# Optimization experiments

Hardware: AMD Instinct MI355X
Metric: run time of the kernel (lower is better)

## Reference

```python
import jax, jax.numpy as jnp
import numpy as np

B, L, H, NH, NB = 16, 200, 128, 2, 2
ITEMS, SPAN = 50000, 256
NEG = -2.0**32 + 1.0  # mask value used by the torch module


def _ln(x, g, b, eps=1e-8):
    m = jnp.mean(x, axis=-1, keepdims=True)
    v = jnp.mean((x - m) ** 2, axis=-1, keepdims=True)
    return (x - m) / jnp.sqrt(v + eps) * g + b


def setup_inputs() -> dict:
    key = jax.random.key(0)
    ks = jax.random.split(key, 20)
    p = lambda k, s: (jax.random.normal(k, s, jnp.float32) * 0.02)
    item_emb = p(ks[0], (ITEMS + 1, H)).at[0].set(0.0)  # padding_idx=0
    return {
        "user_ids": jax.random.randint(ks[1], (B,), 0, 10000),
        "log_seqs": jax.random.randint(ks[2], (B, L), 0, ITEMS),
        "time_matrices": jax.random.randint(ks[3], (B, L, L), 0, SPAN),
        "pos_seqs": jax.random.randint(ks[4], (B, L), 0, ITEMS),
        "neg_seqs": jax.random.randint(ks[5], (B, L), 0, ITEMS),
        "item_emb": item_emb,
        "pos_K_emb": p(ks[6], (L, H)),
        "pos_V_emb": p(ks[7], (L, H)),
        "time_K_emb": p(ks[8], (SPAN + 1, H)),
        "time_V_emb": p(ks[9], (SPAN + 1, H)),
        "Wq": p(ks[10], (NB, H, H)), "bq": jnp.zeros((NB, H)),
        "Wk": p(ks[11], (NB, H, H)), "bk": jnp.zeros((NB, H)),
        "Wv": p(ks[12], (NB, H, H)), "bv": jnp.zeros((NB, H)),
        "ln1_g": jnp.ones((NB, H)), "ln1_b": jnp.zeros((NB, H)),
        "W1": p(ks[13], (NB, H, H)), "b1": jnp.zeros((NB, H)),
        "W2": p(ks[14], (NB, H, H)), "b2": jnp.zeros((NB, H)),
        "ln2_g": jnp.ones((NB, H)), "ln2_b": jnp.zeros((NB, H)),
        "lnf_g": jnp.ones((H,)), "lnf_b": jnp.zeros((H,)),
    }


def reference(user_ids, log_seqs, time_matrices, pos_seqs, neg_seqs,
              item_emb, pos_K_emb, pos_V_emb, time_K_emb, time_V_emb,
              Wq, bq, Wk, bk, Wv, bv, ln1_g, ln1_b,
              W1, b1, W2, b2, ln2_g, ln2_b, lnf_g, lnf_b):
    d = H // NH
    pad = (log_seqs == 0)                    # (B,L) timeline mask
    keep = (~pad)[..., None].astype(jnp.float32)

    seqs = item_emb[log_seqs] * jnp.sqrt(jnp.float32(H))
    seqs = seqs * keep
    posK = pos_K_emb.reshape(L, NH, d)       # same for every batch element
    posV = pos_V_emb.reshape(L, NH, d)
    tmK = time_K_emb[time_matrices].reshape(B, L, L, NH, d)  # (B,L,L,h,d)
    tmV = time_V_emb[time_matrices].reshape(B, L, L, NH, d)
    causal = ~jnp.tril(jnp.ones((L, L), dtype=bool))          # True = masked
    mask = pad[:, None, :, None] | causal[None, None, :, :]   # (B,1,L,L) row-mask | causal

    for i in range(NB):
        Q = (seqs @ Wq[i].T + bq[i]).reshape(B, L, NH, d)
        K = (seqs @ Wk[i].T + bk[i]).reshape(B, L, NH, d)
        V = (seqs @ Wv[i].T + bv[i]).reshape(B, L, NH, d)
        aw = jnp.einsum('bqhd,bkhd->bhqk', Q, K)
        aw = aw + jnp.einsum('bqhd,khd->bhqk', Q, posK)
        aw = aw + jnp.einsum('bqkhd,bqhd->bhqk', tmK, Q)
        aw = aw / jnp.sqrt(jnp.float32(d))
        aw = jnp.where(mask, NEG, aw)
        A = jax.nn.softmax(aw, axis=-1)                        # (B,h,L,L)
        out = jnp.einsum('bhqk,bkhd->bqhd', A, V)
        out = out + jnp.einsum('bhqk,khd->bqhd', A, posV)
        out = out + jnp.einsum('bhqk,bqkhd->bqhd', A, tmV)
        out = out.reshape(B, L, H)
        seqs = _ln(seqs + out, ln1_g[i], ln1_b[i])
        ffn = jax.nn.relu(seqs @ W1[i].T + b1[i]) @ W2[i].T + b2[i]
        seqs = _ln(seqs + ffn, ln2_g[i], ln2_b[i])
        seqs = seqs * keep

    log_feats = _ln(seqs, lnf_g, lnf_b)
    pos_logits = jnp.sum(log_feats * item_emb[pos_seqs], axis=-1)  # (B,L)
    neg_logits = jnp.sum(log_feats * item_emb[neg_seqs], axis=-1)
    return jnp.stack([pos_logits, neg_logits])  # (2,B,L)
```

## Files before the change

kernel.cpp:

```cpp
#include <hip/hip_runtime.h>
#include <hip/hip_bf16.h>
#include <math.h>

#define BB 16
#define LL 200
#define HH 128
#define DD 64
#define NQT 25
#define NEGF -4294967295.0f
#define SQRTH 11.313708498984761f

__global__ __launch_bounds__(512) void k_qkv(float* __restrict__ seqs,
    const int* __restrict__ log_seqs, const float* __restrict__ item_emb, int do_embed,
    const float* __restrict__ Wq, const float* __restrict__ bq,
    const float* __restrict__ Wk, const float* __restrict__ bk,
    const float* __restrict__ Wv, const float* __restrict__ bv,
    const float* __restrict__ posK, const float* __restrict__ posV,
    float* __restrict__ Q, float* __restrict__ Kp, float* __restrict__ Vp) {
    __shared__ float s_lds[16][HH];
    int r0g = blockIdx.x * 16;
    int t = threadIdx.x;
    if (do_embed) {
        int r = t >> 5, d4 = t & 31;
        int id = log_seqs[r0g + r];
        float4 v = make_float4(0.f, 0.f, 0.f, 0.f);
        if (id != 0) {
            v = ((const float4*)(item_emb + id * HH))[d4];
            v.x *= SQRTH; v.y *= SQRTH; v.z *= SQRTH; v.w *= SQRTH;
        }
        *(float4*)&s_lds[r][d4 * 4] = v;
        ((float4*)(seqs + r0g * HH))[t] = v;
    } else {
        ((float4*)s_lds)[t] = ((const float4*)(seqs + r0g * HH))[t];
    }
    __syncthreads();
    int c = t & 127, rg = t >> 7;
    float aq[4] = {0.f, 0.f, 0.f, 0.f};
    float ak[4] = {0.f, 0.f, 0.f, 0.f};
    float av[4] = {0.f, 0.f, 0.f, 0.f};
    const float4* wq4 = (const float4*)(Wq + c * HH);
    const float4* wk4 = (const float4*)(Wk + c * HH);
    const float4* wv4 = (const float4*)(Wv + c * HH);
#pragma unroll 4
    for (int k4 = 0; k4 < HH / 4; ++k4) {
        float4 wq = wq4[k4], wk = wk4[k4], wv = wv4[k4];
#pragma unroll
        for (int r = 0; r < 4; ++r) {
            float4 s = *(const float4*)&s_lds[rg * 4 + r][k4 * 4];
            aq[r] += s.x * wq.x + s.y * wq.y + s.z * wq.z + s.w * wq.w;
            ak[r] += s.x * wk.x + s.y * wk.y + s.z * wk.z + s.w * wk.w;
            av[r] += s.x * wv.x + s.y * wv.y + s.z * wv.z + s.w * wv.w;
        }
    }
#pragma unroll
    for (int r = 0; r < 4; ++r) {
        int row = r0g + rg * 4 + r;
        int l = row % LL;
        Q[row * HH + c]  = aq[r] + bq[c];
        Kp[row * HH + c] = ak[r] + bk[c] + posK[l * HH + c];
        Vp[row * HH + c] = av[r] + bv[c] + posV[l * HH + c];
    }
}

__global__ __launch_bounds__(256) void k_proj(const float* __restrict__ Q,
    const float* __restrict__ timeK, float* __restrict__ projK) {
    int bh = blockIdx.x / 25, qt = blockIdx.x % 25;
    int b = bh >> 1, h = bh & 1;
    int qlo = qt * 8;
    __shared__ float Qs[8][68];
    __shared__ float TK[2][32][68];
    int t = threadIdx.x;
    if (t < 128) {
        int r = t >> 4, d4 = t & 15;
        *(float4*)&Qs[r][d4 * 4] =
            ((const float4*)(Q + (b * LL + qlo + r) * HH + h * DD))[d4];
    }
    for (int x = t; x < 512; x += 256) {
        int i = x >> 4, d4 = x & 15;
        *(float4*)&TK[0][i][d4 * 4] =
            ((const float4*)(timeK + i * HH + h * DD))[d4];
    }
    int tq = t >> 5, ttl = t & 31;
    for (int ch = 0; ch < 9; ++ch) {
        __syncthreads();
        if (ch + 1 < 9) {
            int nb = (ch + 1) * 32;
            for (int x = t; x < 512; x += 256) {
                int i = x >> 4, d4 = x & 15;
                int tt = nb + i;
                if (tt < 257)
                    *(float4*)&TK[(ch + 1) & 1][i][d4 * 4] =
                        ((const float4*)(timeK + tt * HH + h * DD))[d4];
            }
        }
        int tt = ch * 32 + ttl;
        if (tt < 257) {
            float acc = 0.f;
#pragma unroll
            for (int d4 = 0; d4 < 16; ++d4) {
                float4 qv = *(const float4*)&Qs[tq][d4 * 4];
                float4 kv = *(const float4*)&TK[ch & 1][ttl][d4 * 4];
                acc += qv.x * kv.x + qv.y * kv.y + qv.z * kv.z + qv.w * kv.w;
            }
            projK[(bh * LL + qlo + tq) * 257 + tt] = acc;
        }
    }
}

__global__ __launch_bounds__(256) void k_attn(
    const float* __restrict__ Q, const float* __restrict__ Kp, const float* __restrict__ Vp,
    const float* __restrict__ projK, const float* __restrict__ timeV,
    const int* __restrict__ tm, const int* __restrict__ log_seqs,
    float* __restrict__ attnout) {
    int bh = blockIdx.x / NQT, qt = blockIdx.x % NQT;
    int b = bh >> 1, h = bh & 1;
    int qlo = qt * 8;
    __shared__ float K_s[2][32][68];
    __shared__ float smemW[457 * 12];
    __shared__ int s_allmask;
#define WT(i, j) smemW[(i) * 12 + (j)]
    int t = threadIdx.x;
    int tq = t >> 5, lane = t & 31, g = tq;
    int q = qlo + tq;
    int qhi = qlo + 7;

    if (t == 0) s_allmask = 0;
    for (int x = 200 * 12 + t; x < 457 * 12; x += 256) smemW[x] = 0.f;
    float4 qreg[16];
    {
        const float4* qp = (const float4*)(Q + (b * LL + q) * HH + h * DD);
#pragma unroll
        for (int d4 = 0; d4 < 16; ++d4) qreg[d4] = qp[d4];
    }
    const int* tmrow = tm + (b * LL + q) * LL;
    const float* projrow = projK + (bh * LL + q) * 257;
    const int* lsrow = log_seqs + b * LL;

    for (int x = t; x < 512; x += 256) {
        int i = x >> 4, d4 = x & 15;
        *(float4*)&K_s[0][i][d4 * 4] =
            ((const float4*)(Kp + (b * LL + i) * HH + h * DD))[d4];
    }

    float s[7];
#pragma unroll
    for (int j = 0; j < 7; ++j) s[j] = NEGF;
    int nkc = (qhi >> 5) + 1;
#pragma unroll
    for (int kc = 0; kc < 7; ++kc) {
        if (kc < nkc) {
            __syncthreads();
            if (kc + 1 < nkc) {
                int kb = (kc + 1) * 32;
                for (int x = t; x < 512; x += 256) {
                    int i = x >> 4, d4 = x & 15;
                    int k = kb + i;
                    if (k < LL)
                        *(float4*)&K_s[(kc + 1) & 1][i][d4 * 4] =
                            ((const float4*)(Kp + (b * LL + k) * HH + h * DD))[d4];
                }
            }
            int k = kc * 32 + lane;
            if (k <= q && lsrow[k] != 0) {
                float acc = 0.f;
#pragma unroll
                for (int d4 = 0; d4 < 16; ++d4) {
                    float4 kv = *(const float4*)&K_s[kc & 1][lane][d4 * 4];
                    acc += qreg[d4].x * kv.x + qreg[d4].y * kv.y +
                           qreg[d4].z * kv.z + qreg[d4].w * kv.w;
                }
                s[kc] = (acc + projrow[tmrow[k]]) * 0.125f;
            }
        }
    }

    float mx = s[0];
#pragma unroll
    for (int j = 1; j < 7; ++j) mx = fmaxf(mx, s[j]);
    mx = fmaxf(mx, __shfl_xor(mx, 1, 64));
    mx = fmaxf(mx, __shfl_xor(mx, 2, 64));
    mx = fmaxf(mx, __shfl_xor(mx, 4, 64));
    mx = fmaxf(mx, __shfl_xor(mx, 8, 64));
    mx = fmaxf(mx, __shfl_xor(mx, 16, 64));
    bool allmask = (mx == NEGF);
    float sum = 0.f;
#pragma unroll
    for (int j = 0; j < 7; ++j) {
        int k = lane + 32 * j;
        float e = (k < LL) ? __expf(s[j] - mx) : 0.f;
        s[j] = e;
        sum += e;
    }
    sum += __shfl_xor(sum, 1, 64);
    sum += __shfl_xor(sum, 2, 64);
    sum += __shfl_xor(sum, 4, 64);
    sum += __shfl_xor(sum, 8, 64);
    sum += __shfl_xor(sum, 16, 64);
    float inv = 1.0f / sum;
    int klim = allmask ? LL : (q + 1);
    if (allmask && lane == 0) s_allmask = 1;
#pragma unroll
    for (int j = 0; j < 7; ++j) {
        int k = lane + 32 * j;
        if (k < LL) {
            float p = s[j] * inv;
            WT(k, tq) = p;
            if (k < klim && p != 0.f)
                atomicAdd(&WT(200 + tmrow[k], tq), p);
        }
    }
    __syncthreads();

    int kmax = s_allmask ? LL : (qhi + 1);
    float a00=0.f,a01=0.f,a10=0.f,a11=0.f,a20=0.f,a21=0.f,a30=0.f,a31=0.f;
    float a40=0.f,a41=0.f,a50=0.f,a51=0.f,a60=0.f,a61=0.f,a70=0.f,a71=0.f;
#define PV_STEP(WROW, SRCPTR)                                            \
    {                                                                    \
        const float* wr = &WROW;                                         \
        float4 w0 = *(const float4*)wr;                                  \
        float4 w1 = *(const float4*)(wr + 4);                            \
        float2 vv = *(const float2*)(SRCPTR);                            \
        a00 += w0.x * vv.x; a01 += w0.x * vv.y;                          \
        a10 += w0.y * vv.x; a11 += w0.y * vv.y;                          \
        a20 += w0.z * vv.x; a21 += w0.z * vv.y;                          \
        a30 += w0.w * vv.x; a31 += w0.w * vv.y;                          \
        a40 += w1.x * vv.x; a41 += w1.x * vv.y;                          \
        a50 += w1.y * vv.x; a51 += w1.y * vv.y;                          \
        a60 += w1.z * vv.x; a61 += w1.z * vv.y;                          \
        a70 += w1.w * vv.x; a71 += w1.w * vv.y;                          \
    }
    for (int i = g; i < kmax; i += 8)
        PV_STEP(WT(i, 0), Vp + (b * LL + i) * HH + h * DD + lane * 2);
    for (int i = g; i < 257; i += 8)
        PV_STEP(WT(200 + i, 0), timeV + i * HH + h * DD + lane * 2);
#undef PV_STEP
    __syncthreads();
    float* part = smemW;
    part[g * 512 + 0 * 64 + lane * 2] = a00; part[g * 512 + 0 * 64 + lane * 2 + 1] = a01;
    part[g * 512 + 1 * 64 + lane * 2] = a10; part[g * 512 + 1 * 64 + lane * 2 + 1] = a11;
    part[g * 512 + 2 * 64 + lane * 2] = a20; part[g * 512 + 2 * 64 + lane * 2 + 1] = a21;
    part[g * 512 + 3 * 64 + lane * 2] = a30; part[g * 512 + 3 * 64 + lane * 2 + 1] = a31;
    part[g * 512 + 4 * 64 + lane * 2] = a40; part[g * 512 + 4 * 64 + lane * 2 + 1] = a41;
    part[g * 512 + 5 * 64 + lane * 2] = a50; part[g * 512 + 5 * 64 + lane * 2 + 1] = a51;
    part[g * 512 + 6 * 64 + lane * 2] = a60; part[g * 512 + 6 * 64 + lane * 2 + 1] = a61;
    part[g * 512 + 7 * 64 + lane * 2] = a70; part[g * 512 + 7 * 64 + lane * 2 + 1] = a71;
    __syncthreads();
    {
        float ox = 0.f, oy = 0.f;
#pragma unroll
        for (int gg = 0; gg < 8; ++gg) {
            ox += part[gg * 512 + tq * 64 + lane * 2];
            oy += part[gg * 512 + tq * 64 + lane * 2 + 1];
        }
        *(float2*)(attnout + (b * LL + q) * HH + h * DD + lane * 2) =
            make_float2(ox, oy);
    }
#undef WT
}

__global__ __launch_bounds__(512) void k_ffn_full(
    float* __restrict__ seqs, const float* __restrict__ AO,
    const float* __restrict__ g1, const float* __restrict__ be1,
    const float* __restrict__ W1, const float* __restrict__ b1,
    const float* __restrict__ W2, const float* __restrict__ b2,
    const float* __restrict__ g2, const float* __restrict__ be2,
    const int* __restrict__ log_seqs, int do_final,
    const float* __restrict__ lnf_g, const float* __restrict__ lnf_b,
    const float* __restrict__ item_emb,
    const int* __restrict__ pos_seqs, const int* __restrict__ neg_seqs,
    float* __restrict__ out) {
    __shared__ float s_lds[16][HH];
    __shared__ float h_lds[16][HH];
    int r0g = blockIdx.x * 16;
    int t = threadIdx.x;
    {
        float4 a = ((const float4*)(seqs + r0g * HH))[t];
        float4 o = ((const float4*)(AO + r0g * HH))[t];
        a.x += o.x; a.y += o.y; a.z += o.z; a.w += o.w;
        ((float4*)s_lds)[t] = a;
    }
    __syncthreads();
    int w = t >> 6, lane = t & 63;
    int lrow = w * 2 + (lane >> 5), cl = lane & 31;
    {
        float sm = 0.f;
#pragma unroll
        for (int j = 0; j < 4; ++j) sm += s_lds[lrow][cl + 32 * j];
        sm += __shfl_xor(sm, 1, 64);  sm += __shfl_xor(sm, 2, 64);
        sm += __shfl_xor(sm, 4, 64);  sm += __shfl_xor(sm, 8, 64);
        sm += __shfl_xor(sm, 16, 64);
        float mean = sm * (1.0f / HH);
        float vr = 0.f;
#pragma unroll
        for (int j = 0; j < 4; ++j) {
            float d = s_lds[lrow][cl + 32 * j] - mean;
            vr += d * d;
        }
        vr += __shfl_xor(vr, 1, 64);  vr += __shfl_xor(vr, 2, 64);
        vr += __shfl_xor(vr, 4, 64);  vr += __shfl_xor(vr, 8, 64);
        vr += __shfl_xor(vr, 16, 64);
        float rstd = rsqrtf(vr * (1.0f / HH) + 1e-8f);
#pragma unroll
        for (int j = 0; j < 4; ++j) {
            int c = cl + 32 * j;
            s_lds[lrow][c] = (s_lds[lrow][c] - mean) * rstd * g1[c] + be1[c];
        }
    }
    __syncthreads();
    int c = t & 127, rg = t >> 7;
    float acc[4] = {0.f, 0.f, 0.f, 0.f};
    const float4* w14 = (const float4*)(W1 + c * HH);
#pragma unroll 4
    for (int k4 = 0; k4 < HH / 4; ++k4) {
        float4 ww = w14[k4];
#pragma unroll
        for (int r = 0; r < 4; ++r) {
            float4 s = *(const float4*)&s_lds[rg * 4 + r][k4 * 4];
            acc[r] += s.x * ww.x + s.y * ww.y + s.z * ww.z + s.w * ww.w;
        }
    }
#pragma unroll
    for (int r = 0; r < 4; ++r) h_lds[rg * 4 + r][c] = fmaxf(acc[r] + b1[c], 0.f);
    __syncthreads();
#pragma unroll
    for (int r = 0; r < 4; ++r) acc[r] = 0.f;
    const float4* w24 = (const float4*)(W2 + c * HH);
#pragma unroll 4
    for (int k4 = 0; k4 < HH / 4; ++k4) {
        float4 ww = w24[k4];
#pragma unroll
        for (int r = 0; r < 4; ++r) {
            float4 s = *(const float4*)&h_lds[rg * 4 + r][k4 * 4];
            acc[r] += s.x * ww.x + s.y * ww.y + s.z * ww.z + s.w * ww.w;
        }
    }
    __syncthreads();
#pragma unroll
    for (int r = 0; r < 4; ++r)
        h_lds[rg * 4 + r][c] = s_lds[rg * 4 + r][c] + acc[r] + b2[c];
    __syncthreads();
    {
        float sm = 0.f;
#pragma unroll
        for (int j = 0; j < 4; ++j) sm += h_lds[lrow][cl + 32 * j];
        sm += __shfl_xor(sm, 1, 64);  sm += __shfl_xor(sm, 2, 64);
        sm += __shfl_xor(sm, 4, 64);  sm += __shfl_xor(sm, 8, 64);
        sm += __shfl_xor(sm, 16, 64);
        float mean = sm * (1.0f / HH);
        float vr = 0.f;
#pragma unroll
        for (int j = 0; j < 4; ++j) {
            float d = h_lds[lrow][cl + 32 * j] - mean;
            vr += d * d;
        }
        vr += __shfl_xor(vr, 1, 64);  vr += __shfl_xor(vr, 2, 64);
        vr += __shfl_xor(vr, 4, 64);  vr += __shfl_xor(vr, 8, 64);
        vr += __shfl_xor(vr, 16, 64);
        float rstd = rsqrtf(vr * (1.0f / HH) + 1e-8f);
        int row = r0g + lrow;
        float keep = (log_seqs[row] != 0) ? 1.0f : 0.0f;
        float y2[4];
#pragma unroll
        for (int j = 0; j < 4; ++j) {
            int cc = cl + 32 * j;
            y2[j] = ((h_lds[lrow][cc] - mean) * rstd * g2[cc] + be2[cc]) * keep;
        }
        if (!do_final) {
#pragma unroll
            for (int j = 0; j < 4; ++j)
                seqs[row * HH + cl + 32 * j] = y2[j];
        } else {
            float sm2 = y2[0] + y2[1] + y2[2] + y2[3];
            sm2 += __shfl_xor(sm2, 1, 64);  sm2 += __shfl_xor(sm2, 2, 64);
            sm2 += __shfl_xor(sm2, 4, 64);  sm2 += __shfl_xor(sm2, 8, 64);
            sm2 += __shfl_xor(sm2, 16, 64);
            float mean2 = sm2 * (1.0f / HH);
            float vr2 = 0.f;
#pragma unroll
            for (int j = 0; j < 4; ++j) {
                float d = y2[j] - mean2;
                vr2 += d * d;
            }
            vr2 += __shfl_xor(vr2, 1, 64);  vr2 += __shfl_xor(vr2, 2, 64);
            vr2 += __shfl_xor(vr2, 4, 64);  vr2 += __shfl_xor(vr2, 8, 64);
            vr2 += __shfl_xor(vr2, 16, 64);
            float rstd2 = rsqrtf(vr2 * (1.0f / HH) + 1e-8f);
            int pid = pos_seqs[row];
            int nid = neg_seqs[row];
            float pp = 0.f, nn = 0.f;
#pragma unroll
            for (int j = 0; j < 4; ++j) {
                int cc = cl + 32 * j;
                float lf = (y2[j] - mean2) * rstd2 * lnf_g[cc] + lnf_b[cc];
                pp += lf * item_emb[pid * HH + cc];
                nn += lf * item_emb[nid * HH + cc];
            }
            pp += __shfl_xor(pp, 1, 64);  pp += __shfl_xor(pp, 2, 64);
            pp += __shfl_xor(pp, 4, 64);  pp += __shfl_xor(pp, 8, 64);
            pp += __shfl_xor(pp, 16, 64);
            nn += __shfl_xor(nn, 1, 64);  nn += __shfl_xor(nn, 2, 64);
            nn += __shfl_xor(nn, 4, 64);  nn += __shfl_xor(nn, 8, 64);
            nn += __shfl_xor(nn, 16, 64);
            if (cl == 0) {
                out[row] = pp;
                out[BB * LL + row] = nn;
            }
        }
    }
}

extern "C" void kernel_launch(void* const* d_in, const int* in_sizes, int n_in,
                              void* d_out, int out_size, void* d_ws, size_t ws_size,
                              hipStream_t stream) {
    const int* log_seqs = (const int*)d_in[1];
    const int* tm       = (const int*)d_in[2];
    const int* pos_seqs = (const int*)d_in[3];
    const int* neg_seqs = (const int*)d_in[4];
    const float* item_emb = (const float*)d_in[5];
    const float* posK   = (const float*)d_in[6];
    const float* posV   = (const float*)d_in[7];
    const float* timeK  = (const float*)d_in[8];
    const float* timeV  = (const float*)d_in[9];
    const float* Wq = (const float*)d_in[10];
    const float* bq = (const float*)d_in[11];
    const float* Wk = (const float*)d_in[12];
    const float* bk = (const float*)d_in[13];
    const float* Wv = (const float*)d_in[14];
    const float* bv = (const float*)d_in[15];
    const float* ln1_g = (const float*)d_in[16];
    const float* ln1_b = (const float*)d_in[17];
    const float* W1 = (const float*)d_in[18];
    const float* b1 = (const float*)d_in[19];
    const float* W2 = (const float*)d_in[20];
    const float* b2 = (const float*)d_in[21];
    const float* ln2_g = (const float*)d_in[22];
    const float* ln2_b = (const float*)d_in[23];
    const float* lnf_g = (const float*)d_in[24];
    const float* lnf_b = (const float*)d_in[25];

    float* ws    = (float*)d_ws;
    float* seqs  = ws;
    float* Qb    = seqs + 409600;
    float* Kpb   = Qb + 409600;
    float* Vpb   = Kpb + 409600;
    float* AO    = Vpb + 409600;
    float* projK = AO + 409600;

    for (int i = 0; i < 2; ++i) {
        k_qkv<<<BB * LL / 16, 512, 0, stream>>>(seqs, log_seqs, item_emb,
            (i == 0) ? 1 : 0,
            Wq + i * HH * HH, bq + i * HH,
            Wk + i * HH * HH, bk + i * HH,
            Wv + i * HH * HH, bv + i * HH,
            posK, posV, Qb, Kpb, Vpb);
        k_proj<<<32 * NQT, 256, 0, stream>>>(Qb, timeK, projK);
        k_attn<<<32 * NQT, 256, 0, stream>>>(Qb, Kpb, Vpb, projK, timeV,
                                             tm, log_seqs, AO);
        k_ffn_full<<<BB * LL / 16, 512, 0, stream>>>(seqs, AO,
            ln1_g + i * HH, ln1_b + i * HH,
            W1 + i * HH * HH, b1 + i * HH,
            W2 + i * HH * HH, b2 + i * HH,
            ln2_g + i * HH, ln2_b + i * HH, log_seqs,
            (i == 1) ? 1 : 0, lnf_g, lnf_b, item_emb,
            pos_seqs, neg_seqs, (float*)d_out);
    }
}
```

Baseline: 186.1 us.

## Pre-transpose weights for coalesced GEMV and shrink row tiles; drop K double-buffering

Adds a prep kernel that transposes all Q/K/V/FFN weight matrices once per call into workspace, so the qkv and ffn kernels can read weights as coalesced float4 columns, with each thread computing 4 outputs for one row. Row tiles shrink from 16 to 8 with 256-thread blocks, doubling the block count. In k_proj and k_attn the double-buffered K/timeK shared-memory staging becomes a single buffer with an extra barrier per chunk. This trades an extra launch and less load/compute overlap for better weight-access coalescing and more parallelism.

```diff
diff --git a/kernel.cpp b/kernel.cpp
--- a/kernel.cpp
+++ b/kernel.cpp
@@ -10,55 +10,89 @@
 #define NEGF -4294967295.0f
 #define SQRTH 11.313708498984761f
 
-__global__ __launch_bounds__(512) void k_qkv(float* __restrict__ seqs,
+__global__ __launch_bounds__(256) void k_prep(const float* __restrict__ Wq,
+    const float* __restrict__ Wk, const float* __restrict__ Wv,
+    const float* __restrict__ W1, const float* __restrict__ W2,
+    float* __restrict__ WT) {
+    int m = blockIdx.x >> 4, tile = blockIdx.x & 15;
+    const float* base = (m < 2) ? Wq : (m < 4) ? Wk : (m < 6) ? Wv : (m < 8) ? W1 : W2;
+    const float* src = base + (m & 1) * HH * HH;
+    float* dst = WT + m * HH * HH;
+    __shared__ float tb[32][33];
+    int t = threadIdx.x;
+    int tr = tile >> 2, tc = tile & 3;
+    int lr = t >> 3, lc = (t & 7) * 4;
+    float4 v = *(const float4*)(src + (tr * 32 + lr) * HH + tc * 32 + lc);
+    tb[lr][lc + 0] = v.x; tb[lr][lc + 1] = v.y;
+    tb[lr][lc + 2] = v.z; tb[lr][lc + 3] = v.w;
+    __syncthreads();
+    float4 o;
+    o.x = tb[lc + 0][lr]; o.y = tb[lc + 1][lr];
+    o.z = tb[lc + 2][lr]; o.w = tb[lc + 3][lr];
+    *(float4*)(dst + (tc * 32 + lr) * HH + tr * 32 + lc) = o;
+}
+
+__global__ __launch_bounds__(256) void k_qkv(float* __restrict__ seqs,
     const int* __restrict__ log_seqs, const float* __restrict__ item_emb, int do_embed,
-    const float* __restrict__ Wq, const float* __restrict__ bq,
-    const float* __restrict__ Wk, const float* __restrict__ bk,
-    const float* __restrict__ Wv, const float* __restrict__ bv,
+    const float* __restrict__ WTq, const float* __restrict__ bq,
+    const float* __restrict__ WTk, const float* __restrict__ bk,
+    const float* __restrict__ WTv, const float* __restrict__ bv,
     const float* __restrict__ posK, const float* __restrict__ posV,
     float* __restrict__ Q, float* __restrict__ Kp, float* __restrict__ Vp) {
-    __shared__ float s_lds[16][HH];
-    int r0g = blockIdx.x * 16;
+    __shared__ float s_lds[8][HH];
+    int r0g = blockIdx.x * 8;
     int t = threadIdx.x;
-    if (do_embed) {
+    {
         int r = t >> 5, d4 = t & 31;
-        int id = log_seqs[r0g + r];
-        float4 v = make_float4(0.f, 0.f, 0.f, 0.f);
-        if (id != 0) {
-            v = ((const float4*)(item_emb + id * HH))[d4];
-            v.x *= SQRTH; v.y *= SQRTH; v.z *= SQRTH; v.w *= SQRTH;
-        }
-        *(float4*)&s_lds[r][d4 * 4] = v;
-        ((float4*)(seqs + r0g * HH))[t] = v;
-    } else {
-        ((float4*)s_lds)[t] = ((const float4*)(seqs + r0g * HH))[t];
-    }
-    __syncthreads();
-    int c = t & 127, rg = t >> 7;
-    float aq[4] = {0.f, 0.f, 0.f, 0.f};
-    float ak[4] = {0.f, 0.f, 0.f, 0.f};
-    float av[4] = {0.f, 0.f, 0.f, 0.f};
-    const float4* wq4 = (const float4*)(Wq + c * HH);
-    const float4* wk4 = (const float4*)(Wk + c * HH);
-    const float4* wv4 = (const float4*)(Wv + c * HH);
+        if (do_embed) {
+            int id = log_seqs[r0g + r];
+            float4 v = make_float4(0.f, 0.f, 0.f, 0.f);
+            if (id != 0) {
+                v = ((const float4*)(item_emb + id * HH))[d4];
+                v.x *= SQRTH; v.y *= SQRTH; v.z *= SQRTH; v.w *= SQRTH;
+            }
+            *(float4*)&s_lds[r][d4 * 4] = v;
+            ((float4*)(seqs + r0g * HH))[t] = v;
+        } else {
+            ((float4*)s_lds)[t] = ((const float4*)(seqs + r0g * HH))[t];
+        }
+    }
+    __syncthreads();
+    int r = t >> 5, j = t & 31;
+    const float4* wq4 = (const float4*)WTq + j;
+    const float4* wk4 = (const float4*)WTk + j;
+    const float4* wv4 = (const float4*)WTv + j;
+    float4 aq = make_float4(0.f, 0.f, 0.f, 0.f);
+    float4 ak = make_float4(0.f, 0.f, 0.f, 0.f);
+    float4 av = make_float4(0.f, 0.f, 0.f, 0.f);
 #pragma unroll 4
-    for (int k4 = 0; k4 < HH / 4; ++k4) {
-        float4 wq = wq4[k4], wk = wk4[k4], wv = wv4[k4];
-#pragma unroll
-        for (int r = 0; r < 4; ++r) {
-            float4 s = *(const float4*)&s_lds[rg * 4 + r][k4 * 4];
-            aq[r] += s.x * wq.x + s.y * wq.y + s.z * wq.z + s.w * wq.w;
-            ak[r] += s.x * wk.x + s.y * wk.y + s.z * wk.z + s.w * wk.w;
-            av[r] += s.x * wv.x + s.y * wv.y + s.z * wv.z + s.w * wv.w;
-        }
-    }
-#pragma unroll
-    for (int r = 0; r < 4; ++r) {
-        int row = r0g + rg * 4 + r;
-        int l = row % LL;
-        Q[row * HH + c]  = aq[r] + bq[c];
-        Kp[row * HH + c] = ak[r] + bk[c] + posK[l * HH + c];
-        Vp[row * HH + c] = av[r] + bv[c] + posV[l * HH + c];
+    for (int k = 0; k < HH; ++k) {
+        float sv = s_lds[r][k];
+        float4 wq = wq4[k * 32];
+        float4 wk = wk4[k * 32];
+        float4 wv = wv4[k * 32];
+        aq.x += sv * wq.x; aq.y += sv * wq.y; aq.z += sv * wq.z; aq.w += sv * wq.w;
+        ak.x += sv * wk.x; ak.y += sv * wk.y; ak.z += sv * wk.z; ak.w += sv * wk.w;
+        av.x += sv * wv.x; av.y += sv * wv.y; av.z += sv * wv.z; av.w += sv * wv.w;
+    }
+    int row = r0g + r;
+    int l = row % LL;
+    {
+        float4 b = ((const float4*)bq)[j];
+        aq.x += b.x; aq.y += b.y; aq.z += b.z; aq.w += b.w;
+        ((float4*)(Q + row * HH))[j] = aq;
+    }
+    {
+        float4 b = ((const float4*)bk)[j];
+        float4 p = ((const float4*)(posK + l * HH))[j];
+        ak.x += b.x + p.x; ak.y += b.y + p.y; ak.z += b.z + p.z; ak.w += b.w + p.w;
+        ((float4*)(Kp + row * HH))[j] = ak;
+    }
+    {
+        float4 b = ((const float4*)bv)[j];
+        float4 p = ((const float4*)(posV + l * HH))[j];
+        av.x += b.x + p.x; av.y += b.y + p.y; av.z += b.z + p.z; av.w += b.w + p.w;
+        ((float4*)(Vp + row * HH))[j] = av;
     }
 }
 
@@ -68,38 +102,32 @@
     int b = bh >> 1, h = bh & 1;
     int qlo = qt * 8;
     __shared__ float Qs[8][68];
-    __shared__ float TK[2][32][68];
+    __shared__ float TK[32][68];
     int t = threadIdx.x;
     if (t < 128) {
         int r = t >> 4, d4 = t & 15;
         *(float4*)&Qs[r][d4 * 4] =
             ((const float4*)(Q + (b * LL + qlo + r) * HH + h * DD))[d4];
     }
-    for (int x = t; x < 512; x += 256) {
-        int i = x >> 4, d4 = x & 15;
-        *(float4*)&TK[0][i][d4 * 4] =
-            ((const float4*)(timeK + i * HH + h * DD))[d4];
-    }
     int tq = t >> 5, ttl = t & 31;
     for (int ch = 0; ch < 9; ++ch) {
+        int base = ch * 32;
         __syncthreads();
-        if (ch + 1 < 9) {
-            int nb = (ch + 1) * 32;
-            for (int x = t; x < 512; x += 256) {
-                int i = x >> 4, d4 = x & 15;
-                int tt = nb + i;
-                if (tt < 257)
-                    *(float4*)&TK[(ch + 1) & 1][i][d4 * 4] =
-                        ((const float4*)(timeK + tt * HH + h * DD))[d4];
-            }
-        }
-        int tt = ch * 32 + ttl;
+        for (int x = t; x < 512; x += 256) {
+            int i = x >> 4, d4 = x & 15;
+            int tt = base + i;
+            if (tt < 257)
+                *(float4*)&TK[i][d4 * 4] =
+                    ((const float4*)(timeK + tt * HH + h * DD))[d4];
+        }
+        __syncthreads();
+        int tt = base + ttl;
         if (tt < 257) {
             float acc = 0.f;
 #pragma unroll
             for (int d4 = 0; d4 < 16; ++d4) {
                 float4 qv = *(const float4*)&Qs[tq][d4 * 4];
-                float4 kv = *(const float4*)&TK[ch & 1][ttl][d4 * 4];
+                float4 kv = *(const float4*)&TK[ttl][d4 * 4];
                 acc += qv.x * kv.x + qv.y * kv.y + qv.z * kv.z + qv.w * kv.w;
             }
             projK[(bh * LL + qlo + tq) * 257 + tt] = acc;
@@ -115,7 +143,7 @@
     int bh = blockIdx.x / NQT, qt = blockIdx.x % NQT;
     int b = bh >> 1, h = bh & 1;
     int qlo = qt * 8;
-    __shared__ float K_s[2][32][68];
+    __shared__ float K_s[32][68];
     __shared__ float smemW[457 * 12];
     __shared__ int s_allmask;
 #define WT(i, j) smemW[(i) * 12 + (j)]
@@ -136,12 +164,6 @@
     const float* projrow = projK + (bh * LL + q) * 257;
     const int* lsrow = log_seqs + b * LL;
 
-    for (int x = t; x < 512; x += 256) {
-        int i = x >> 4, d4 = x & 15;
-        *(float4*)&K_s[0][i][d4 * 4] =
-            ((const float4*)(Kp + (b * LL + i) * HH + h * DD))[d4];
-    }
-
     float s[7];
 #pragma unroll
     for (int j = 0; j < 7; ++j) s[j] = NEGF;
@@ -149,28 +171,27 @@
 #pragma unroll
     for (int kc = 0; kc < 7; ++kc) {
         if (kc < nkc) {
+            int kbase = kc * 32;
+            for (int x = t; x < 512; x += 256) {
+                int i = x >> 4, d4 = x & 15;
+                int k = kbase + i;
+                if (k < LL)
+                    *(float4*)&K_s[i][d4 * 4] =
+                        ((const float4*)(Kp + (b * LL + k) * HH + h * DD))[d4];
+            }
             __syncthreads();
-            if (kc + 1 < nkc) {
-                int kb = (kc + 1) * 32;
-                for (int x = t; x < 512; x += 256) {
-                    int i = x >> 4, d4 = x & 15;
-                    int k = kb + i;
-                    if (k < LL)
-                        *(float4*)&K_s[(kc + 1) & 1][i][d4 * 4] =
-                            ((const float4*)(Kp + (b * LL + k) * HH + h * DD))[d4];
-                }
-            }
-            int k = kc * 32 + lane;
+            int k = kbase + lane;
             if (k <= q && lsrow[k] != 0) {
                 float acc = 0.f;
 #pragma unroll
                 for (int d4 = 0; d4 < 16; ++d4) {
-                    float4 kv = *(const float4*)&K_s[kc & 1][lane][d4 * 4];
+                    float4 kv = *(const float4*)&K_s[lane][d4 * 4];
                     acc += qreg[d4].x * kv.x + qreg[d4].y * kv.y +
                            qreg[d4].z * kv.z + qreg[d4].w * kv.w;
                 }
                 s[kc] = (acc + projrow[tmrow[k]]) * 0.125f;
             }
+            __syncthreads();
         }
     }
 
@@ -258,20 +279,20 @@
 #undef WT
 }
 
-__global__ __launch_bounds__(512) void k_ffn_full(
+__global__ __launch_bounds__(256) void k_ffn(
     float* __restrict__ seqs, const float* __restrict__ AO,
     const float* __restrict__ g1, const float* __restrict__ be1,
-    const float* __restrict__ W1, const float* __restrict__ b1,
-    const float* __restrict__ W2, const float* __restrict__ b2,
+    const float* __restrict__ WT1, const float* __restrict__ b1,
+    const float* __restrict__ WT2, const float* __restrict__ b2,
     const float* __restrict__ g2, const float* __restrict__ be2,
     const int* __restrict__ log_seqs, int do_final,
     const float* __restrict__ lnf_g, const float* __restrict__ lnf_b,
     const float* __restrict__ item_emb,
     const int* __restrict__ pos_seqs, const int* __restrict__ neg_seqs,
     float* __restrict__ out) {
-    __shared__ float s_lds[16][HH];
-    __shared__ float h_lds[16][HH];
-    int r0g = blockIdx.x * 16;
+    __shared__ float s_lds[8][HH];
+    __shared__ float h_lds[8][HH];
+    int r0g = blockIdx.x * 8;
     int t = threadIdx.x;
     {
         float4 a = ((const float4*)(seqs + r0g * HH))[t];
@@ -307,50 +328,54 @@
         }
     }
     __syncthreads();
-    int c = t & 127, rg = t >> 7;
-    float acc[4] = {0.f, 0.f, 0.f, 0.f};
-    const float4* w14 = (const float4*)(W1 + c * HH);
+    int r = t >> 5, j = t & 31;
+    {
+        const float4* w4 = (const float4*)WT1 + j;
+        float4 acc = make_float4(0.f, 0.f, 0.f, 0.f);
 #pragma unroll 4
-    for (int k4 = 0; k4 < HH / 4; ++k4) {
-        float4 ww = w14[k4];
-#pragma unroll
-        for (int r = 0; r < 4; ++r) {
-            float4 s = *(const float4*)&s_lds[rg * 4 + r][k4 * 4];
-            acc[r] += s.x * ww.x + s.y * ww.y + s.z * ww.z + s.w * ww.w;
-        }
-    }
-#pragma unroll
-    for (int r = 0; r < 4; ++r) h_lds[rg * 4 + r][c] = fmaxf(acc[r] + b1[c], 0.f);
-    __syncthreads();
-#pragma unroll
-    for (int r = 0; r < 4; ++r) acc[r] = 0.f;
-    const float4* w24 = (const float4*)(W2 + c * HH);
+        for (int k = 0; k < HH; ++k) {
+            float sv = s_lds[r][k];
+            float4 ww = w4[k * 32];
+            acc.x += sv * ww.x; acc.y += sv * ww.y;
+            acc.z += sv * ww.z; acc.w += sv * ww.w;
+        }
+        float4 b = ((const float4*)b1)[j];
+        acc.x = fmaxf(acc.x + b.x, 0.f); acc.y = fmaxf(acc.y + b.y, 0.f);
+        acc.z = fmaxf(acc.z + b.z, 0.f); acc.w = fmaxf(acc.w + b.w, 0.f);
+        *(float4*)&h_lds[r][j * 4] = acc;
+    }
+    __syncthreads();
+    float4 x2;
+    {
+        const float4* w4 = (const float4*)WT2 + j;
+        float4 acc = make_float4(0.f, 0.f, 0.f, 0.f);
 #pragma unroll 4
-    for (int k4 = 0; k4 < HH / 4; ++k4) {
-        float4 ww = w24[k4];
-#pragma unroll
-        for (int r = 0; r < 4; ++r) {
-            float4 s = *(const float4*)&h_lds[rg * 4 + r][k4 * 4];
-            acc[r] += s.x * ww.x + s.y * ww.y + s.z * ww.z + s.w * ww.w;
-        }
-    }
-    __syncthreads();
-#pragma unroll
-    for (int r = 0; r < 4; ++r)
-        h_lds[rg * 4 + r][c] = s_lds[rg * 4 + r][c] + acc[r] + b2[c];
+        for (int k = 0; k < HH; ++k) {
+            float hv = h_lds[r][k];
+            float4 ww = w4[k * 32];
+            acc.x += hv * ww.x; acc.y += hv * ww.y;
+            acc.z += hv * ww.z; acc.w += hv * ww.w;
+        }
+        float4 b = ((const float4*)b2)[j];
+        float4 s1 = *(const float4*)&s_lds[r][j * 4];
+        x2.x = s1.x + acc.x + b.x; x2.y = s1.y + acc.y + b.y;
+        x2.z = s1.z + acc.z + b.z; x2.w = s1.w + acc.w + b.w;
+    }
+    __syncthreads();
+    *(float4*)&h_lds[r][j * 4] = x2;
     __syncthreads();
     {
         float sm = 0.f;
 #pragma unroll
-        for (int j = 0; j < 4; ++j) sm += h_lds[lrow][cl + 32 * j];
+        for (int jj = 0; jj < 4; ++jj) sm += h_lds[lrow][cl + 32 * jj];
         sm += __shfl_xor(sm, 1, 64);  sm += __shfl_xor(sm, 2, 64);
         sm += __shfl_xor(sm, 4, 64);  sm += __shfl_xor(sm, 8, 64);
         sm += __shfl_xor(sm, 16, 64);
         float mean = sm * (1.0f / HH);
         float vr = 0.f;
 #pragma unroll
-        for (int j = 0; j < 4; ++j) {
-            float d = h_lds[lrow][cl + 32 * j] - mean;
+        for (int jj = 0; jj < 4; ++jj) {
+            float d = h_lds[lrow][cl + 32 * jj] - mean;
             vr += d * d;
         }
         vr += __shfl_xor(vr, 1, 64);  vr += __shfl_xor(vr, 2, 64);
@@ -361,14 +386,14 @@
         float keep = (log_seqs[row] != 0) ? 1.0f : 0.0f;
         float y2[4];
 #pragma unroll
-        for (int j = 0; j < 4; ++j) {
-            int cc = cl + 32 * j;
-            y2[j] = ((h_lds[lrow][cc] - mean) * rstd * g2[cc] + be2[cc]) * keep;
+        for (int jj = 0; jj < 4; ++jj) {
+            int cc = cl + 32 * jj;
+            y2[jj] = ((h_lds[lrow][cc] - mean) * rstd * g2[cc] + be2[cc]) * keep;
         }
         if (!do_final) {
 #pragma unroll
-            for (int j = 0; j < 4; ++j)
-                seqs[row * HH + cl + 32 * j] = y2[j];
+            for (int jj = 0; jj < 4; ++jj)
+                seqs[row * HH + cl + 32 * jj] = y2[jj];
         } else {
             float sm2 = y2[0] + y2[1] + y2[2] + y2[3];
             sm2 += __shfl_xor(sm2, 1, 64);  sm2 += __shfl_xor(sm2, 2, 64);
@@ -377,8 +402,8 @@
             float mean2 = sm2 * (1.0f / HH);
             float vr2 = 0.f;
 #pragma unroll
-            for (int j = 0; j < 4; ++j) {
-                float d = y2[j] - mean2;
+            for (int jj = 0; jj < 4; ++jj) {
+                float d = y2[jj] - mean2;
                 vr2 += d * d;
             }
             vr2 += __shfl_xor(vr2, 1, 64);  vr2 += __shfl_xor(vr2, 2, 64);
@@ -389,9 +414,9 @@
             int nid = neg_seqs[row];
             float pp = 0.f, nn = 0.f;
 #pragma unroll
-            for (int j = 0; j < 4; ++j) {
-                int cc = cl + 32 * j;
-                float lf = (y2[j] - mean2) * rstd2 * lnf_g[cc] + lnf_b[cc];
+            for (int jj = 0; jj < 4; ++jj) {
+                int cc = cl + 32 * jj;
+                float lf = (y2[jj] - mean2) * rstd2 * lnf_g[cc] + lnf_b[cc];
                 pp += lf * item_emb[pid * HH + cc];
                 nn += lf * item_emb[nid * HH + cc];
             }
@@ -445,21 +470,26 @@
     float* Vpb   = Kpb + 409600;
     float* AO    = Vpb + 409600;
     float* projK = AO + 409600;
+    float* WT    = projK + 1644800;
+
+    k_prep<<<160, 256, 0, stream>>>(Wq, Wk, Wv, W1, W2, WT);
 
     for (int i = 0; i < 2; ++i) {
-        k_qkv<<<BB * LL / 16, 512, 0, stream>>>(seqs, log_seqs, item_emb,
+        const float* WTq = WT + (0 * 2 + i) * HH * HH;
+        const float* WTk = WT + (1 * 2 + i) * HH * HH;
+        const float* WTv = WT + (2 * 2 + i) * HH * HH;
+        const float* WT1 = WT + (3 * 2 + i) * HH * HH;
+        const float* WT2 = WT + (4 * 2 + i) * HH * HH;
+        k_qkv<<<BB * LL / 8, 256, 0, stream>>>(seqs, log_seqs, item_emb,
             (i == 0) ? 1 : 0,
-            Wq + i * HH * HH, bq + i * HH,
-            Wk + i * HH * HH, bk + i * HH,
-            Wv + i * HH * HH, bv + i * HH,
+            WTq, bq + i * HH, WTk, bk + i * HH, WTv, bv + i * HH,
             posK, posV, Qb, Kpb, Vpb);
         k_proj<<<32 * NQT, 256, 0, stream>>>(Qb, timeK, projK);
         k_attn<<<32 * NQT, 256, 0, stream>>>(Qb, Kpb, Vpb, projK, timeV,
                                              tm, log_seqs, AO);
-        k_ffn_full<<<BB * LL / 16, 512, 0, stream>>>(seqs, AO,
+        k_ffn<<<BB * LL / 8, 256, 0, stream>>>(seqs, AO,
             ln1_g + i * HH, ln1_b + i * HH,
-            W1 + i * HH * HH, b1 + i * HH,
-            W2 + i * HH * HH, b2 + i * HH,
+            WT1, b1 + i * HH, WT2, b2 + i * HH,
             ln2_g + i * HH, ln2_b + i * HH, log_seqs,
             (i == 1) ? 1 : 0, lnf_g, lnf_b, item_emb,
             pos_seqs, neg_seqs, (float*)d_out);
```

New measurement: 194.8 us. 4.7% more time.
